# Kernel optimization log

Measured on AMD Instinct MI355X. Metric: run time of the kernel, lower is better.

Reference implementation:

```python
import jax, jax.numpy as jnp
import numpy as np
from jax import lax

B, NC, NF = 16, 1024, 4096   # clouds, coarse pts/cloud, fine pts/cloud
C_IN, C_SKIP, C_HID, K = 256, 128, 256, 3
BN_EPS = 1e-5


def setup_inputs() -> dict:
    key = jax.random.key(0)
    ks = jax.random.split(key, 12)
    inp = {
        "x": jax.random.normal(ks[0], (B * NC, C_IN), jnp.float32),
        "pos": jax.random.normal(ks[1], (B * NC, 3), jnp.float32),
        "batch": jnp.arange(B * NC, dtype=jnp.int64) // NC,
        "x_skip": jax.random.normal(ks[2], (B * NF, C_SKIP), jnp.float32),
        "pos_skip": jax.random.normal(ks[3], (B * NF, 3), jnp.float32),
        "batch_skip": jnp.arange(B * NF, dtype=jnp.int64) // NF,
    }
    d_in = C_IN + C_SKIP
    inp["W1"] = jax.random.normal(ks[4], (d_in, C_HID), jnp.float32) / np.sqrt(d_in)
    inp["b1"] = jnp.zeros((C_HID,), jnp.float32)
    inp["g1"] = jnp.ones((C_HID,), jnp.float32)
    inp["be1"] = jnp.zeros((C_HID,), jnp.float32)
    inp["W2"] = jax.random.normal(ks[5], (C_HID, C_HID), jnp.float32) / np.sqrt(C_HID)
    inp["b2"] = jnp.zeros((C_HID,), jnp.float32)
    inp["g2"] = jnp.ones((C_HID,), jnp.float32)
    inp["be2"] = jnp.zeros((C_HID,), jnp.float32)
    return inp


def _knn_interpolate(x, pos, pos_skip):
    # batches are contiguous equal-size -> reshape per cloud
    xb = x.reshape(B, NC, C_IN)
    pc = pos.reshape(B, NC, 3)
    pf = pos_skip.reshape(B, NF, 3)
    # squared distances [B, NF, NC]
    d2 = jnp.sum((pf[:, :, None, :] - pc[:, None, :, :]) ** 2, axis=-1)
    neg_d, idx = lax.top_k(-d2, K)                      # [B, NF, K]
    w = 1.0 / jnp.maximum(-neg_d, 1e-16)                # inverse-squared-distance weights
    feats = xb[jnp.arange(B)[:, None, None], idx]       # [B, NF, K, C_IN]
    out = jnp.sum(w[..., None] * feats, axis=2) / jnp.sum(w, axis=2, keepdims=True)
    return out.reshape(B * NF, C_IN)


def _mlp_layer(h, W, b, g, be):
    z = jax.nn.relu(h @ W + b)
    mean = jnp.mean(z, axis=0)
    var = jnp.mean((z - mean) ** 2, axis=0)            # biased var, as torch BN
    return (z - mean) * lax.rsqrt(var + BN_EPS) * g + be


def reference(x, pos, batch, x_skip, pos_skip, batch_skip,
              W1, b1, g1, be1, W2, b2, g2, be2):
    h = _knn_interpolate(x, pos, pos_skip)
    h = jnp.concatenate([h, x_skip], axis=1)            # [B*NF, C_IN+C_SKIP]
    h = _mlp_layer(h, W1, b1, g1, be1)
    h = _mlp_layer(h, W2, b2, g2, be2)
    return h
```

## Files before the change

### kernel.cpp

```cpp
#include <hip/hip_runtime.h>
#include <hip/hip_bf16.h>

#define NB    16
#define NC    1024
#define NF    4096
#define MROWS 65536
#define CIN   256
#define CSK   128
#define DIN   384
#define CHID  256
#define BN_EPS 1e-5f

typedef __attribute__((ext_vector_type(8))) short bf16x8;
typedef __attribute__((ext_vector_type(4))) float f32x4;

__device__ __forceinline__ unsigned short f2bfu(float f) {
  __hip_bfloat16 h = __float2bfloat16(f);
  return __builtin_bit_cast(unsigned short, h);
}
__device__ __forceinline__ float bfu2f(unsigned short u) {
  unsigned int w = ((unsigned int)u) << 16;
  return __builtin_bit_cast(float, w);
}
__device__ __forceinline__ unsigned int pack2(float lo, float hi) {
  return ((unsigned int)f2bfu(hi) << 16) | (unsigned int)f2bfu(lo);
}

__device__ __forceinline__ void load_lds16(const void* g, void* lds) {
  __builtin_amdgcn_global_load_lds(
      (const __attribute__((address_space(1))) unsigned int*)g,
      (__attribute__((address_space(3))) unsigned int*)lds, 16, 0, 0);
}

__device__ __forceinline__ void ins3(float d2, int j, float& b0, float& b1,
                                     float& b2v, int& i0, int& i1, int& i2) {
  const bool c0 = d2 < b0, c1 = d2 < b1, c2 = d2 < b2v;
  const float nb1 = __builtin_amdgcn_fmed3f(d2, b0, b1);
  const float nb2 = __builtin_amdgcn_fmed3f(d2, b1, b2v);
  i2  = c1 ? i1 : (c2 ? j : i2);
  i1  = c0 ? i0 : (c1 ? j : i1);
  i0  = c0 ? j : i0;
  b2v = nb2;
  b1  = nb1;
  b0  = fminf(d2, b0);
}

__device__ __forceinline__ void ins3tb(float d, int j, float& b0, float& b1,
                                       float& b2v, int& i0, int& i1, int& i2) {
  const bool c0 = (d < b0) || (d == b0 && j < i0);
  const bool c1 = (d < b1) || (d == b1 && j < i1);
  const bool c2 = (d < b2v) || (d == b2v && j < i2);
  const float nb1 = __builtin_amdgcn_fmed3f(d, b0, b1);
  const float nb2 = __builtin_amdgcn_fmed3f(d, b1, b2v);
  i2  = c1 ? i1 : (c2 ? j : i2);
  i1  = c0 ? i0 : (c1 ? j : i1);
  i0  = c0 ? j : i0;
  b2v = nb2;
  b1  = nb1;
  b0  = fminf(d, b0);
}

__global__ __launch_bounds__(256) void knn_interp_kernel(
    const float* __restrict__ x,
    const float* __restrict__ pos,
    const float* __restrict__ x_skip,
    const float* __restrict__ pos_skip,
    __hip_bfloat16* __restrict__ h0,
    const float* __restrict__ W1,
    __hip_bfloat16* __restrict__ W1t,
    float* __restrict__ stats)
{
  const int tid = threadIdx.x, lane = tid & 63, wid = tid >> 6;

  if (blockIdx.x >= 2048) {
    const int c = blockIdx.x - 2048;
    if (c == 0) {
      for (int k = tid; k < 1024; k += 256) stats[k] = 0.f;
    }
    W1t[(size_t)tid * DIN + c] = __float2bfloat16(W1[(size_t)c * CHID + tid]);
    return;
  }

  __shared__ float4 cposI[NC];

  const int f0 = blockIdx.x * 32;
  const int b  = f0 >> 12;

  const float* pb = pos + (size_t)b * NC * 3;
  for (int j = tid; j < NC; j += 256) {
    const int slot = ((j & 127) << 3) | ((j >> 7) ^ (j & 7));
    cposI[slot] = make_float4(pb[3 * j], pb[3 * j + 1], pb[3 * j + 2], 0.f);
  }
  __syncthreads();

  const int ll = lane & 7;
  const int pl = wid * 8 + (lane >> 3);
  const int f  = f0 + pl;
  const float fx = pos_skip[(size_t)f * 3];
  const float fy = pos_skip[(size_t)f * 3 + 1];
  const float fz = pos_skip[(size_t)f * 3 + 2];
  const int jb = ll * 128;

  float a0 = 3.4e38f, a1 = 3.4e38f, a2 = 3.4e38f;
  float c0 = 3.4e38f, c1 = 3.4e38f, c2 = 3.4e38f;
  int ia0 = 0, ia1 = 0, ia2 = 0, ic0 = 0, ic1 = 0, ic2 = 0;
#pragma unroll 8
  for (int t = 0; t < 64; ++t) {
    const int sw = ll ^ (t & 7);
    const float4 pA = cposI[t * 8 + sw];
    const float4 pB = cposI[(t + 64) * 8 + sw];
    const float dxA = __fsub_rn(fx, pA.x), dyA = __fsub_rn(fy, pA.y),
                dzA = __fsub_rn(fz, pA.z);
    const float dxB = __fsub_rn(fx, pB.x), dyB = __fsub_rn(fy, pB.y),
                dzB = __fsub_rn(fz, pB.z);
    const float d2A = __fadd_rn(
        __fadd_rn(__fmul_rn(dxA, dxA), __fmul_rn(dyA, dyA)),
        __fmul_rn(dzA, dzA));
    const float d2B = __fadd_rn(
        __fadd_rn(__fmul_rn(dxB, dxB), __fmul_rn(dyB, dyB)),
        __fmul_rn(dzB, dzB));
    ins3(d2A, jb + t,      a0, a1, a2, ia0, ia1, ia2);
    ins3(d2B, jb + 64 + t, c0, c1, c2, ic0, ic1, ic2);
  }
  ins3(c0, ic0, a0, a1, a2, ia0, ia1, ia2);
  ins3(c1, ic1, a0, a1, a2, ia0, ia1, ia2);
  ins3(c2, ic2, a0, a1, a2, ia0, ia1, ia2);

#pragma unroll
  for (int mm = 1; mm <= 4; mm <<= 1) {
    const float o0 = __shfl_xor(a0, mm);
    const float o1 = __shfl_xor(a1, mm);
    const float o2 = __shfl_xor(a2, mm);
    const int oj0 = __shfl_xor(ia0, mm);
    const int oj1 = __shfl_xor(ia1, mm);
    const int oj2 = __shfl_xor(ia2, mm);
    ins3tb(o0, oj0, a0, a1, a2, ia0, ia1, ia2);
    ins3tb(o1, oj1, a0, a1, a2, ia0, ia1, ia2);
    ins3tb(o2, oj2, a0, a1, a2, ia0, ia1, ia2);
  }

  float w0 = 1.f / fmaxf(a0, 1e-16f);
  float w1 = 1.f / fmaxf(a1, 1e-16f);
  float w2 = 1.f / fmaxf(a2, 1e-16f);
  const float inv = 1.f / (w0 + w1 + w2);
  w0 *= inv; w1 *= inv; w2 *= inv;

  const float4* r0 = (const float4*)(x + (size_t)(b * NC + ia0) * CIN);
  const float4* r1 = (const float4*)(x + (size_t)(b * NC + ia1) * CIN);
  const float4* r2 = (const float4*)(x + (size_t)(b * NC + ia2) * CIN);
  __hip_bfloat16* orow = h0 + (size_t)f * DIN;
  unsigned int* o2u = (unsigned int*)orow;
#pragma unroll
  for (int k = 0; k < 8; ++k) {
    const int fi4 = k * 8 + ll;
    const float4 A = r0[fi4], B = r1[fi4], C = r2[fi4];
    float4 v;
    v.x = w0 * A.x + w1 * B.x + w2 * C.x;
    v.y = w0 * A.y + w1 * B.y + w2 * C.y;
    v.z = w0 * A.z + w1 * B.z + w2 * C.z;
    v.w = w0 * A.w + w1 * B.w + w2 * C.w;
    uint2 o;
    o.x = pack2(v.x, v.y);
    o.y = pack2(v.z, v.w);
    ((uint2*)o2u)[fi4] = o;
  }
  const float4* xs = (const float4*)(x_skip + (size_t)f * CSK);
  unsigned int* o2s = (unsigned int*)(orow + CIN);
#pragma unroll
  for (int k = 0; k < 4; ++k) {
    const int fi4 = k * 8 + ll;
    const float4 s = xs[fi4];
    uint2 o;
    o.x = pack2(s.x, s.y);
    o.y = pack2(s.z, s.w);
    ((uint2*)o2s)[fi4] = o;
  }
}

__global__ __launch_bounds__(256) void prep_w2b2_kernel(
    const float* __restrict__ W2, const float* __restrict__ stats,
    const float* __restrict__ g1, const float* __restrict__ be1,
    const float* __restrict__ b2, __hip_bfloat16* __restrict__ W2t,
    float* __restrict__ b2p) {
  const int n = blockIdx.x, c = threadIdx.x;
  const int wid = c >> 6, lane = c & 63;
  const float m = stats[c] * (1.f / MROWS);
  const float var = stats[256 + c] * (1.f / MROWS) - m * m;
  const float sc = g1[c] * rsqrtf(var + BN_EPS);
  const float sh = be1[c] - m * sc;
  const float w = W2[(size_t)c * CHID + n];
  W2t[(size_t)n * CHID + c] = __float2bfloat16(sc * w);
  float p = sh * w;
#pragma unroll
  for (int off = 32; off > 0; off >>= 1) p += __shfl_down(p, off);
  __shared__ float red4[4];
  if (lane == 0) red4[wid] = p;
  __syncthreads();
  if (c == 0) b2p[n] = red4[0] + red4[1] + red4[2] + red4[3] + b2[n];
}

template<int KD>
__global__ __launch_bounds__(512) void gemm_bias_relu(
    const __hip_bfloat16* __restrict__ A,
    const __hip_bfloat16* __restrict__ Bt,
    const float* __restrict__ bias,
    __hip_bfloat16* __restrict__ out,
    float* __restrict__ gsum,
    float* __restrict__ gsq)
{
  __shared__ __hip_bfloat16 As[2 * 128 * 32];
  __shared__ __hip_bfloat16 Bs[2 * 256 * 32];
  __shared__ float ssum[256], ssq[256];
  const int tid = threadIdx.x;
  const int wid = tid >> 6, lane = tid & 63;
  const int bm = blockIdx.x;
  const int wr = wid >> 2, wc = wid & 3;
  const int la = lane & 15, lk = lane >> 4;

  if (tid < 256) { ssum[tid] = 0.f; ssq[tid] = 0.f; }

  f32x4 acc[4][4] = {};

  const int rA = tid >> 2;
  const int c8 = (tid & 3) * 8;
  const __hip_bfloat16* gA  = A  + (size_t)(bm * 128 + rA) * KD + c8;
  const __hip_bfloat16* gB0 = Bt + (size_t)rA * KD + c8;
  const __hip_bfloat16* gB1 = Bt + (size_t)(128 + rA) * KD + c8;
  char* ldsA  = (char*)As + wid * 1024;
  char* ldsB0 = (char*)Bs + wid * 1024;

  load_lds16(gA,  ldsA);
  load_lds16(gB0, ldsB0);
  load_lds16(gB1, ldsB0 + 8192);
  __syncthreads();

  const int nIter = KD / 32;
  for (int it = 0; it < nIter; ++it) {
    const int cur = it & 1, nxt = cur ^ 1;
    if (it + 1 < nIter) {
      const int k1 = (it + 1) * 32;
      load_lds16(gA  + k1, ldsA  + nxt * 8192);
      load_lds16(gB0 + k1, ldsB0 + nxt * 16384);
      load_lds16(gB1 + k1, ldsB0 + nxt * 16384 + 8192);
    }
    const __hip_bfloat16* Acur = As + cur * 4096;
    const __hip_bfloat16* Bcur = Bs + cur * 8192;
    bf16x8 af[4], bfr[4];
#pragma unroll
    for (int m = 0; m < 4; ++m)
      af[m] = *(const bf16x8*)(Acur + (wr * 64 + m * 16 + la) * 32 + lk * 8);
#pragma unroll
    for (int n = 0; n < 4; ++n)
      bfr[n] = *(const bf16x8*)(Bcur + (wc * 64 + n * 16 + la) * 32 + lk * 8);
#pragma unroll
    for (int m = 0; m < 4; ++m)
#pragma unroll
      for (int n = 0; n < 4; ++n)
        acc[m][n] = __builtin_amdgcn_mfma_f32_16x16x32_bf16(
            af[m], bfr[n], acc[m][n], 0, 0, 0);
    __syncthreads();
  }

  const int rowBase = bm * 128 + wr * 64 + lk * 4;
#pragma unroll
  for (int n = 0; n < 4; ++n) {
    const int col = wc * 64 + n * 16 + la;
    const float bs = bias[col];
    float ls = 0.f, ls2 = 0.f;
#pragma unroll
    for (int m = 0; m < 4; ++m) {
      const int row = rowBase + m * 16;
#pragma unroll
      for (int j = 0; j < 4; ++j) {
        float v = acc[m][n][j] + bs;
        v = fmaxf(v, 0.f);
        ls += v; ls2 += v * v;
        out[(size_t)(row + j) * 256 + col] = __float2bfloat16(v);
      }
    }
    atomicAdd(&ssum[col], ls);
    atomicAdd(&ssq[col], ls2);
  }
  __syncthreads();
  if (tid < 256) {
    atomicAdd(&gsum[tid], ssum[tid]);
    atomicAdd(&gsq[tid], ssq[tid]);
  }
}

__global__ __launch_bounds__(256) void bn_apply_kernel(
    const __hip_bfloat16* __restrict__ Z, const float* __restrict__ stats,
    const float* __restrict__ g2, const float* __restrict__ be2,
    float* __restrict__ out) {
  __shared__ float ssc[256], ssh[256];
  const int t = threadIdx.x;
  {
    const float m = stats[t] * (1.f / MROWS);
    const float var = stats[256 + t] * (1.f / MROWS) - m * m;
    const float sc = g2[t] * rsqrtf(var + BN_EPS);
    ssc[t] = sc;
    ssh[t] = be2[t] - m * sc;
  }
  __syncthreads();
  const size_t i8 = (size_t)blockIdx.x * 256 + t;
  const uint4 raw = ((const uint4*)Z)[i8];
  const int c0 = (int)((i8 * 8) & 255);
  const float4 scA = *(const float4*)(ssc + c0);
  const float4 scB = *(const float4*)(ssc + c0 + 4);
  const float4 shA = *(const float4*)(ssh + c0);
  const float4 shB = *(const float4*)(ssh + c0 + 4);
  float4 oa, ob;
  oa.x = bfu2f((unsigned short)(raw.x & 0xffff)) * scA.x + shA.x;
  oa.y = bfu2f((unsigned short)(raw.x >> 16))    * scA.y + shA.y;
  oa.z = bfu2f((unsigned short)(raw.y & 0xffff)) * scA.z + shA.z;
  oa.w = bfu2f((unsigned short)(raw.y >> 16))    * scA.w + shA.w;
  ob.x = bfu2f((unsigned short)(raw.z & 0xffff)) * scB.x + shB.x;
  ob.y = bfu2f((unsigned short)(raw.z >> 16))    * scB.y + shB.y;
  ob.z = bfu2f((unsigned short)(raw.w & 0xffff)) * scB.z + shB.z;
  ob.w = bfu2f((unsigned short)(raw.w >> 16))    * scB.w + shB.w;
  ((float4*)(out))[i8 * 2]     = oa;
  ((float4*)(out))[i8 * 2 + 1] = ob;
}

extern "C" void kernel_launch(void* const* d_in, const int* in_sizes, int n_in,
                              void* d_out, int out_size, void* d_ws,
                              size_t ws_size, hipStream_t stream) {
  (void)in_sizes; (void)n_in; (void)out_size; (void)ws_size;
  const float* x        = (const float*)d_in[0];
  const float* pos      = (const float*)d_in[1];
  const float* x_skip   = (const float*)d_in[3];
  const float* pos_skip = (const float*)d_in[4];
  const float* W1  = (const float*)d_in[6];
  const float* b1  = (const float*)d_in[7];
  const float* g1  = (const float*)d_in[8];
  const float* be1 = (const float*)d_in[9];
  const float* W2  = (const float*)d_in[10];
  const float* b2  = (const float*)d_in[11];
  const float* g2  = (const float*)d_in[12];
  const float* be2 = (const float*)d_in[13];
  float* out = (float*)d_out;

  char* ws = (char*)d_ws;
  __hip_bfloat16* h0  = (__hip_bfloat16*)(ws);
  __hip_bfloat16* z2  = (__hip_bfloat16*)(ws);
  __hip_bfloat16* W1t = (__hip_bfloat16*)(ws + 50331648);
  __hip_bfloat16* z1  = (__hip_bfloat16*)(ws + 50528256);
  __hip_bfloat16* W2t = (__hip_bfloat16*)(ws + 84082688);
  float* b2p    = (float*)(ws + 84213760);
  float* stats  = (float*)(ws + 84214784);

  knn_interp_kernel<<<2432, 256, 0, stream>>>(x, pos, x_skip, pos_skip, h0,
                                              W1, W1t, stats);
  gemm_bias_relu<DIN><<<512, 512, 0, stream>>>(h0, W1t, b1, z1,
                                               stats, stats + 256);
  prep_w2b2_kernel<<<256, 256, 0, stream>>>(W2, stats, g1, be1, b2, W2t, b2p);
  gemm_bias_relu<CHID><<<512, 512, 0, stream>>>(z1, W2t, b2p, z2,
                                                stats + 512, stats + 768);
  bn_apply_kernel<<<8192, 256, 0, stream>>>(z2, stats + 512, g2, be2, out);
}
```

Measured before the change: 133.3 us.

## Project coarse features through W1 before interpolation and fuse gather into skip GEMM

Interpolation is linear, so the coarse features x are multiplied by the first 256 rows of W1 at coarse resolution (16K rows instead of 64K). The fine-resolution GEMM then only covers the 128 skip channels. The KNN scan now writes weights and indices to a small record buffer. The skip GEMM kernel gathers and blends the three projected coarse rows into LDS and adds them before bias and ReLU. This removes most of the layer-1 GEMM FLOPs and the wide h0 round-trip, at the cost of an extra fp32 y buffer, gather traffic, and bf16 rounding of the interpolated projections, which is numerically different from the reference order.

Result: slower. 161.2 us (+20.9%).

```diff
diff --git a/kernel.cpp b/kernel.cpp
--- a/kernel.cpp
+++ b/kernel.cpp
@@ -60,120 +60,296 @@
   b0  = fminf(d, b0);
 }
 
-__global__ __launch_bounds__(256) void knn_interp_kernel(
-    const float* __restrict__ x,
-    const float* __restrict__ pos,
-    const float* __restrict__ x_skip,
-    const float* __restrict__ pos_skip,
-    __hip_bfloat16* __restrict__ h0,
-    const float* __restrict__ W1,
-    __hip_bfloat16* __restrict__ W1t,
-    float* __restrict__ stats)
-{
+__global__ __launch_bounds__(256) void prep1_kernel(
+    const float* __restrict__ x, const float* __restrict__ W1,
+    __hip_bfloat16* __restrict__ xb, __hip_bfloat16* __restrict__ W1at,
+    float* __restrict__ stats) {
+  const int tid = threadIdx.x, blk = blockIdx.x;
+  if (blk < 1024) {
+    const size_t base = (size_t)blk * 4096 + (size_t)tid * 16;
+    const float4* src = (const float4*)(x + base);
+    const float4 a = src[0], b = src[1], c = src[2], d = src[3];
+    uint4 u1, u2;
+    u1.x = pack2(a.x, a.y); u1.y = pack2(a.z, a.w);
+    u1.z = pack2(b.x, b.y); u1.w = pack2(b.z, b.w);
+    u2.x = pack2(c.x, c.y); u2.y = pack2(c.z, c.w);
+    u2.z = pack2(d.x, d.y); u2.w = pack2(d.z, d.w);
+    uint4* dst = (uint4*)(xb + base);
+    dst[0] = u1; dst[1] = u2;
+  } else if (blk < 1280) {
+    const int k = blk - 1024;
+    W1at[(size_t)tid * 256 + k] = __float2bfloat16(W1[(size_t)k * CHID + tid]);
+  } else {
+    for (int q = tid; q < 1024; q += 256) stats[q] = 0.f;
+  }
+}
+
+__global__ __launch_bounds__(512, 4) void scan_gemmB_kernel(
+    const float* __restrict__ pos, const float* __restrict__ pos_skip,
+    const float* __restrict__ x_skip, const float* __restrict__ W1,
+    const __hip_bfloat16* __restrict__ xb,
+    const __hip_bfloat16* __restrict__ W1at,
+    __hip_bfloat16* __restrict__ xsb, __hip_bfloat16* __restrict__ W1bt,
+    float4* __restrict__ recA, int2* __restrict__ recB,
+    float* __restrict__ y) {
+  __shared__ __align__(16) char smem[49152];
   const int tid = threadIdx.x, lane = tid & 63, wid = tid >> 6;
-
-  if (blockIdx.x >= 2048) {
-    const int c = blockIdx.x - 2048;
-    if (c == 0) {
-      for (int k = tid; k < 1024; k += 256) stats[k] = 0.f;
-    }
-    W1t[(size_t)tid * DIN + c] = __float2bfloat16(W1[(size_t)c * CHID + tid]);
+  const int blk = blockIdx.x;
+
+  if (blk < 1024) {
+    float4* cposI = (float4*)smem;
+    const int f0 = blk * 64;
+    const int b = f0 >> 12;
+    const float* pb = pos + (size_t)b * NC * 3;
+    for (int j = tid; j < NC; j += 512) {
+      const int slot = ((j & 127) << 3) | ((j >> 7) ^ (j & 7));
+      cposI[slot] = make_float4(pb[3 * j], pb[3 * j + 1], pb[3 * j + 2], 0.f);
+    }
+    __syncthreads();
+
+    const int ll = lane & 7;
+    const int pl = wid * 8 + (lane >> 3);
+    const int f = f0 + pl;
+    const float fx = pos_skip[(size_t)f * 3];
+    const float fy = pos_skip[(size_t)f * 3 + 1];
+    const float fz = pos_skip[(size_t)f * 3 + 2];
+    const int jb = ll * 128;
+
+    float a0 = 3.4e38f, a1 = 3.4e38f, a2 = 3.4e38f;
+    float c0 = 3.4e38f, c1 = 3.4e38f, c2 = 3.4e38f;
+    int ia0 = 0, ia1 = 0, ia2 = 0, ic0 = 0, ic1 = 0, ic2 = 0;
+#pragma unroll 8
+    for (int t = 0; t < 64; ++t) {
+      const int sw = ll ^ (t & 7);
+      const float4 pA = cposI[t * 8 + sw];
+      const float4 pB = cposI[(t + 64) * 8 + sw];
+      const float dxA = __fsub_rn(fx, pA.x), dyA = __fsub_rn(fy, pA.y),
+                  dzA = __fsub_rn(fz, pA.z);
+      const float dxB = __fsub_rn(fx, pB.x), dyB = __fsub_rn(fy, pB.y),
+                  dzB = __fsub_rn(fz, pB.z);
+      const float d2A = __fadd_rn(
+          __fadd_rn(__fmul_rn(dxA, dxA), __fmul_rn(dyA, dyA)),
+          __fmul_rn(dzA, dzA));
+      const float d2B = __fadd_rn(
+          __fadd_rn(__fmul_rn(dxB, dxB), __fmul_rn(dyB, dyB)),
+          __fmul_rn(dzB, dzB));
+      ins3(d2A, jb + t,      a0, a1, a2, ia0, ia1, ia2);
+      ins3(d2B, jb + 64 + t, c0, c1, c2, ic0, ic1, ic2);
+    }
+    ins3(c0, ic0, a0, a1, a2, ia0, ia1, ia2);
+    ins3(c1, ic1, a0, a1, a2, ia0, ia1, ia2);
+    ins3(c2, ic2, a0, a1, a2, ia0, ia1, ia2);
+
+#pragma unroll
+    for (int mm = 1; mm <= 4; mm <<= 1) {
+      const float o0 = __shfl_xor(a0, mm);
+      const float o1 = __shfl_xor(a1, mm);
+      const float o2 = __shfl_xor(a2, mm);
+      const int oj0 = __shfl_xor(ia0, mm);
+      const int oj1 = __shfl_xor(ia1, mm);
+      const int oj2 = __shfl_xor(ia2, mm);
+      ins3tb(o0, oj0, a0, a1, a2, ia0, ia1, ia2);
+      ins3tb(o1, oj1, a0, a1, a2, ia0, ia1, ia2);
+      ins3tb(o2, oj2, a0, a1, a2, ia0, ia1, ia2);
+    }
+
+    if (ll == 0) {
+      float w0 = 1.f / fmaxf(a0, 1e-16f);
+      float w1 = 1.f / fmaxf(a1, 1e-16f);
+      float w2 = 1.f / fmaxf(a2, 1e-16f);
+      const float inv = 1.f / (w0 + w1 + w2);
+      recA[f] = make_float4(w0 * inv, w1 * inv, w2 * inv,
+                            __int_as_float(ia0));
+      recB[f] = make_int2(ia1, ia2);
+    }
     return;
   }
 
-  __shared__ float4 cposI[NC];
-
-  const int f0 = blockIdx.x * 32;
-  const int b  = f0 >> 12;
-
-  const float* pb = pos + (size_t)b * NC * 3;
-  for (int j = tid; j < NC; j += 256) {
-    const int slot = ((j & 127) << 3) | ((j >> 7) ^ (j & 7));
-    cposI[slot] = make_float4(pb[3 * j], pb[3 * j + 1], pb[3 * j + 2], 0.f);
-  }
+  if (blk < 1152) {
+    const int bm = blk - 1024;
+    const int wr = wid >> 2, wc = wid & 3;
+    const int la = lane & 15, lk = lane >> 4;
+    f32x4 acc[4][4] = {};
+    const int rA = tid >> 2;
+    const int c8 = (tid & 3) * 8;
+    const __hip_bfloat16* gA  = xb   + (size_t)(bm * 128 + rA) * 256 + c8;
+    const __hip_bfloat16* gB0 = W1at + (size_t)rA * 256 + c8;
+    const __hip_bfloat16* gB1 = W1at + (size_t)(128 + rA) * 256 + c8;
+    char* ldsA  = smem + wid * 1024;
+    char* ldsB0 = smem + 16384 + wid * 1024;
+
+    load_lds16(gA,  ldsA);
+    load_lds16(gB0, ldsB0);
+    load_lds16(gB1, ldsB0 + 8192);
+    __syncthreads();
+
+    for (int it = 0; it < 8; ++it) {
+      const int cur = it & 1, nxt = cur ^ 1;
+      if (it < 7) {
+        const int k1 = (it + 1) * 32;
+        load_lds16(gA  + k1, smem + nxt * 8192 + wid * 1024);
+        load_lds16(gB0 + k1, smem + 16384 + nxt * 16384 + wid * 1024);
+        load_lds16(gB1 + k1, smem + 16384 + nxt * 16384 + wid * 1024 + 8192);
+      }
+      const __hip_bfloat16* Acur = (const __hip_bfloat16*)smem + cur * 4096;
+      const __hip_bfloat16* Bcur =
+          (const __hip_bfloat16*)(smem + 16384) + cur * 8192;
+      bf16x8 af[4], bfr[4];
+#pragma unroll
+      for (int m = 0; m < 4; ++m)
+        af[m] = *(const bf16x8*)(Acur + (wr * 64 + m * 16 + la) * 32 + lk * 8);
+#pragma unroll
+      for (int n = 0; n < 4; ++n)
+        bfr[n] = *(const bf16x8*)(Bcur + (wc * 64 + n * 16 + la) * 32 + lk * 8);
+#pragma unroll
+      for (int m = 0; m < 4; ++m)
+#pragma unroll
+        for (int n = 0; n < 4; ++n)
+          acc[m][n] = __builtin_amdgcn_mfma_f32_16x16x32_bf16(
+              af[m], bfr[n], acc[m][n], 0, 0, 0);
+      __syncthreads();
+    }
+
+    const int rowBase = bm * 128 + wr * 64 + lk * 4;
+#pragma unroll
+    for (int n = 0; n < 4; ++n) {
+      const int col = wc * 64 + n * 16 + la;
+#pragma unroll
+      for (int m = 0; m < 4; ++m)
+#pragma unroll
+        for (int j = 0; j < 4; ++j)
+          y[(size_t)(rowBase + m * 16 + j) * 256 + col] = acc[m][n][j];
+    }
+    return;
+  }
+
+  if (blk < 3200) {
+    const size_t base = (size_t)(blk - 1152) * 4096 + (size_t)tid * 8;
+    const float4* src = (const float4*)(x_skip + base);
+    const float4 a = src[0], b4 = src[1];
+    uint4 u;
+    u.x = pack2(a.x, a.y);  u.y = pack2(a.z, a.w);
+    u.z = pack2(b4.x, b4.y); u.w = pack2(b4.z, b4.w);
+    *(uint4*)(xsb + base) = u;
+    return;
+  }
+
+  {
+    const int q = blk - 3200;
+    const int n = q * 4 + (tid >> 7);
+    const int k = tid & 127;
+    W1bt[(size_t)n * 128 + k] =
+        __float2bfloat16(W1[(size_t)(256 + k) * CHID + n]);
+  }
+}
+
+__global__ __launch_bounds__(512, 4) void gemm_skip_interp_kernel(
+    const __hip_bfloat16* __restrict__ xsb,
+    const __hip_bfloat16* __restrict__ W1bt,
+    const float* __restrict__ b1, const float4* __restrict__ recA,
+    const int2* __restrict__ recB, const float* __restrict__ y,
+    __hip_bfloat16* __restrict__ z1, float* __restrict__ gsum,
+    float* __restrict__ gsq) {
+  __shared__ __hip_bfloat16 As[2 * 64 * 32];
+  __shared__ __hip_bfloat16 Bs[2 * 256 * 32];
+  __shared__ unsigned short itp[64 * 256];
+  __shared__ float lw[64][3];
+  __shared__ int lj[64][3];
+  __shared__ float ssum[256], ssq[256];
+  const int tid = threadIdx.x, lane = tid & 63, wid = tid >> 6;
+  const int bm = blockIdx.x;
+  const int bb = (bm * 64) >> 12;
+
+  if (tid < 256) { ssum[tid] = 0.f; ssq[tid] = 0.f; }
+  if (tid < 64) {
+    const float4 ra = recA[bm * 64 + tid];
+    const int2 rb = recB[bm * 64 + tid];
+    lw[tid][0] = ra.x; lw[tid][1] = ra.y; lw[tid][2] = ra.z;
+    lj[tid][0] = __float_as_int(ra.w); lj[tid][1] = rb.x; lj[tid][2] = rb.y;
+  }
+
+  const int rA = tid >> 2, c8 = (tid & 3) * 8;
+  const __hip_bfloat16* gA  = xsb + (size_t)(bm * 64 + rA) * 128 + c8;
+  const __hip_bfloat16* gB0 = W1bt + (size_t)rA * 128 + c8;
+  const __hip_bfloat16* gB1 = W1bt + (size_t)(128 + rA) * 128 + c8;
+  char* ldsB0 = (char*)Bs + wid * 1024;
+  if (tid < 256) load_lds16(gA, (char*)As + wid * 1024);
+  load_lds16(gB0, ldsB0);
+  load_lds16(gB1, ldsB0 + 8192);
   __syncthreads();
 
-  const int ll = lane & 7;
-  const int pl = wid * 8 + (lane >> 3);
-  const int f  = f0 + pl;
-  const float fx = pos_skip[(size_t)f * 3];
-  const float fy = pos_skip[(size_t)f * 3 + 1];
-  const float fz = pos_skip[(size_t)f * 3 + 2];
-  const int jb = ll * 128;
-
-  float a0 = 3.4e38f, a1 = 3.4e38f, a2 = 3.4e38f;
-  float c0 = 3.4e38f, c1 = 3.4e38f, c2 = 3.4e38f;
-  int ia0 = 0, ia1 = 0, ia2 = 0, ic0 = 0, ic1 = 0, ic2 = 0;
-#pragma unroll 8
-  for (int t = 0; t < 64; ++t) {
-    const int sw = ll ^ (t & 7);
-    const float4 pA = cposI[t * 8 + sw];
-    const float4 pB = cposI[(t + 64) * 8 + sw];
-    const float dxA = __fsub_rn(fx, pA.x), dyA = __fsub_rn(fy, pA.y),
-                dzA = __fsub_rn(fz, pA.z);
-    const float dxB = __fsub_rn(fx, pB.x), dyB = __fsub_rn(fy, pB.y),
-                dzB = __fsub_rn(fz, pB.z);
-    const float d2A = __fadd_rn(
-        __fadd_rn(__fmul_rn(dxA, dxA), __fmul_rn(dyA, dyA)),
-        __fmul_rn(dzA, dzA));
-    const float d2B = __fadd_rn(
-        __fadd_rn(__fmul_rn(dxB, dxB), __fmul_rn(dyB, dyB)),
-        __fmul_rn(dzB, dzB));
-    ins3(d2A, jb + t,      a0, a1, a2, ia0, ia1, ia2);
-    ins3(d2B, jb + 64 + t, c0, c1, c2, ic0, ic1, ic2);
-  }
-  ins3(c0, ic0, a0, a1, a2, ia0, ia1, ia2);
-  ins3(c1, ic1, a0, a1, a2, ia0, ia1, ia2);
-  ins3(c2, ic2, a0, a1, a2, ia0, ia1, ia2);
-
-#pragma unroll
-  for (int mm = 1; mm <= 4; mm <<= 1) {
-    const float o0 = __shfl_xor(a0, mm);
-    const float o1 = __shfl_xor(a1, mm);
-    const float o2 = __shfl_xor(a2, mm);
-    const int oj0 = __shfl_xor(ia0, mm);
-    const int oj1 = __shfl_xor(ia1, mm);
-    const int oj2 = __shfl_xor(ia2, mm);
-    ins3tb(o0, oj0, a0, a1, a2, ia0, ia1, ia2);
-    ins3tb(o1, oj1, a0, a1, a2, ia0, ia1, ia2);
-    ins3tb(o2, oj2, a0, a1, a2, ia0, ia1, ia2);
-  }
-
-  float w0 = 1.f / fmaxf(a0, 1e-16f);
-  float w1 = 1.f / fmaxf(a1, 1e-16f);
-  float w2 = 1.f / fmaxf(a2, 1e-16f);
-  const float inv = 1.f / (w0 + w1 + w2);
-  w0 *= inv; w1 *= inv; w2 *= inv;
-
-  const float4* r0 = (const float4*)(x + (size_t)(b * NC + ia0) * CIN);
-  const float4* r1 = (const float4*)(x + (size_t)(b * NC + ia1) * CIN);
-  const float4* r2 = (const float4*)(x + (size_t)(b * NC + ia2) * CIN);
-  __hip_bfloat16* orow = h0 + (size_t)f * DIN;
-  unsigned int* o2u = (unsigned int*)orow;
-#pragma unroll
-  for (int k = 0; k < 8; ++k) {
-    const int fi4 = k * 8 + ll;
-    const float4 A = r0[fi4], B = r1[fi4], C = r2[fi4];
+  for (int rr = 0; rr < 8; ++rr) {
+    const int r = wid * 8 + rr;
+    const float w0 = lw[r][0], w1 = lw[r][1], w2 = lw[r][2];
+    const float4* y0 = (const float4*)(y + (size_t)(bb * NC + lj[r][0]) * 256);
+    const float4* y1 = (const float4*)(y + (size_t)(bb * NC + lj[r][1]) * 256);
+    const float4* y2 = (const float4*)(y + (size_t)(bb * NC + lj[r][2]) * 256);
+    const float4 A4 = y0[lane], B4 = y1[lane], C4 = y2[lane];
     float4 v;
-    v.x = w0 * A.x + w1 * B.x + w2 * C.x;
-    v.y = w0 * A.y + w1 * B.y + w2 * C.y;
-    v.z = w0 * A.z + w1 * B.z + w2 * C.z;
-    v.w = w0 * A.w + w1 * B.w + w2 * C.w;
+    v.x = w0 * A4.x + w1 * B4.x + w2 * C4.x;
+    v.y = w0 * A4.y + w1 * B4.y + w2 * C4.y;
+    v.z = w0 * A4.z + w1 * B4.z + w2 * C4.z;
+    v.w = w0 * A4.w + w1 * B4.w + w2 * C4.w;
     uint2 o;
     o.x = pack2(v.x, v.y);
     o.y = pack2(v.z, v.w);
-    ((uint2*)o2u)[fi4] = o;
-  }
-  const float4* xs = (const float4*)(x_skip + (size_t)f * CSK);
-  unsigned int* o2s = (unsigned int*)(orow + CIN);
-#pragma unroll
-  for (int k = 0; k < 4; ++k) {
-    const int fi4 = k * 8 + ll;
-    const float4 s = xs[fi4];
-    uint2 o;
-    o.x = pack2(s.x, s.y);
-    o.y = pack2(s.z, s.w);
-    ((uint2*)o2s)[fi4] = o;
+    *(uint2*)((char*)itp + r * 512 + lane * 8) = o;
+  }
+
+  const int wr = wid >> 2, wc = wid & 3;
+  const int la = lane & 15, lk = lane >> 4;
+  f32x4 acc[2][4] = {};
+  for (int it = 0; it < 4; ++it) {
+    const int cur = it & 1, nxt = cur ^ 1;
+    if (it < 3) {
+      const int k1 = (it + 1) * 32;
+      if (tid < 256) load_lds16(gA + k1, (char*)As + nxt * 4096 + wid * 1024);
+      load_lds16(gB0 + k1, (char*)Bs + nxt * 16384 + wid * 1024);
+      load_lds16(gB1 + k1, (char*)Bs + nxt * 16384 + wid * 1024 + 8192);
+    }
+    const __hip_bfloat16* Acur = As + cur * 2048;
+    const __hip_bfloat16* Bcur = Bs + cur * 8192;
+    bf16x8 af[2], bfr[4];
+#pragma unroll
+    for (int m = 0; m < 2; ++m)
+      af[m] = *(const bf16x8*)(Acur + (wr * 32 + m * 16 + la) * 32 + lk * 8);
+#pragma unroll
+    for (int n = 0; n < 4; ++n)
+      bfr[n] = *(const bf16x8*)(Bcur + (wc * 64 + n * 16 + la) * 32 + lk * 8);
+#pragma unroll
+    for (int m = 0; m < 2; ++m)
+#pragma unroll
+      for (int n = 0; n < 4; ++n)
+        acc[m][n] = __builtin_amdgcn_mfma_f32_16x16x32_bf16(
+            af[m], bfr[n], acc[m][n], 0, 0, 0);
+    __syncthreads();
+  }
+
+  const int rowTop = bm * 64;
+#pragma unroll
+  for (int n = 0; n < 4; ++n) {
+    const int col = wc * 64 + n * 16 + la;
+    const float bs = b1[col];
+    float ls = 0.f, ls2 = 0.f;
+#pragma unroll
+    for (int m = 0; m < 2; ++m) {
+#pragma unroll
+      for (int j = 0; j < 4; ++j) {
+        const int lr = wr * 32 + m * 16 + lk * 4 + j;
+        const float iv = bfu2f(itp[lr * 256 + col]);
+        float v = acc[m][n][j] + bs + iv;
+        v = fmaxf(v, 0.f);
+        ls += v; ls2 += v * v;
+        z1[(size_t)(rowTop + lr) * 256 + col] = __float2bfloat16(v);
+      }
+    }
+    atomicAdd(&ssum[col], ls);
+    atomicAdd(&ssq[col], ls2);
+  }
+  __syncthreads();
+  if (tid < 256) {
+    atomicAdd(&gsum[tid], ssum[tid]);
+    atomicAdd(&gsq[tid], ssq[tid]);
   }
 }
 
@@ -201,13 +377,9 @@
 
 template<int KD>
 __global__ __launch_bounds__(512) void gemm_bias_relu(
-    const __hip_bfloat16* __restrict__ A,
-    const __hip_bfloat16* __restrict__ Bt,
-    const float* __restrict__ bias,
-    __hip_bfloat16* __restrict__ out,
-    float* __restrict__ gsum,
-    float* __restrict__ gsq)
-{
+    const __hip_bfloat16* __restrict__ A, const __hip_bfloat16* __restrict__ Bt,
+    const float* __restrict__ bias, __hip_bfloat16* __restrict__ out,
+    float* __restrict__ gsum, float* __restrict__ gsq) {
   __shared__ __hip_bfloat16 As[2 * 128 * 32];
   __shared__ __hip_bfloat16 Bs[2 * 256 * 32];
   __shared__ float ssum[256], ssq[256];
@@ -341,18 +513,24 @@
   float* out = (float*)d_out;
 
   char* ws = (char*)d_ws;
-  __hip_bfloat16* h0  = (__hip_bfloat16*)(ws);
-  __hip_bfloat16* z2  = (__hip_bfloat16*)(ws);
-  __hip_bfloat16* W1t = (__hip_bfloat16*)(ws + 50331648);
-  __hip_bfloat16* z1  = (__hip_bfloat16*)(ws + 50528256);
-  __hip_bfloat16* W2t = (__hip_bfloat16*)(ws + 84082688);
-  float* b2p    = (float*)(ws + 84213760);
-  float* stats  = (float*)(ws + 84214784);
-
-  knn_interp_kernel<<<2432, 256, 0, stream>>>(x, pos, x_skip, pos_skip, h0,
-                                              W1, W1t, stats);
-  gemm_bias_relu<DIN><<<512, 512, 0, stream>>>(h0, W1t, b1, z1,
-                                               stats, stats + 256);
+  __hip_bfloat16* xb   = (__hip_bfloat16*)(ws);
+  __hip_bfloat16* z2   = (__hip_bfloat16*)(ws);
+  __hip_bfloat16* xsb  = (__hip_bfloat16*)(ws + 8388608);
+  float*          y    = (float*)(ws + 25165824);
+  __hip_bfloat16* z1   = (__hip_bfloat16*)(ws + 41943040);
+  __hip_bfloat16* W1at = (__hip_bfloat16*)(ws + 75497472);
+  __hip_bfloat16* W1bt = (__hip_bfloat16*)(ws + 75628544);
+  __hip_bfloat16* W2t  = (__hip_bfloat16*)(ws + 75694080);
+  float4*         recA = (float4*)(ws + 75825152);
+  int2*           recB = (int2*)(ws + 76873728);
+  float*          b2p  = (float*)(ws + 77398016);
+  float*          stats= (float*)(ws + 77399040);
+
+  prep1_kernel<<<1281, 256, 0, stream>>>(x, W1, xb, W1at, stats);
+  scan_gemmB_kernel<<<3264, 512, 0, stream>>>(pos, pos_skip, x_skip, W1, xb,
+                                              W1at, xsb, W1bt, recA, recB, y);
+  gemm_skip_interp_kernel<<<1024, 512, 0, stream>>>(xsb, W1bt, b1, recA, recB,
+                                                    y, z1, stats, stats + 256);
   prep_w2b2_kernel<<<256, 256, 0, stream>>>(W2, stats, g1, be1, b2, W2t, b2p);
   gemm_bias_relu<CHID><<<512, 512, 0, stream>>>(z1, W2t, b2p, z2,
                                                 stats + 512, stats + 768);
```
